# Kernel optimization log

Measured on AMD Instinct MI355X. Metric: run time of the kernel, lower is better.

Reference implementation:

```python
import jax, jax.numpy as jnp
import numpy as np
from jax import lax

D = 1024      # embed_dim
L = 8         # num_blocks
H = 8         # num_heads
P = 4         # patch_size
IMG = 64
B = 64
N = (IMG // P) ** 2 + 1   # 257 tokens (cls + patches)
DF = 4 * D
EPS = 1e-6


def _ln(x, g, b):
    m = jnp.mean(x, axis=-1, keepdims=True)
    v = jnp.var(x, axis=-1, keepdims=True)
    return (x - m) * jax.lax.rsqrt(v + EPS) * g + b


def setup_inputs() -> dict:
    key = jax.random.key(0)
    ks = jax.random.split(key, 20)
    s = 0.02
    return {
        "x": jax.random.normal(ks[0], (B, IMG, IMG, 3), jnp.float32),
        "conv_w": jax.random.normal(ks[1], (P, P, 3, D), jnp.float32) * s,
        "conv_b": jnp.zeros((D,), jnp.float32),
        "cls_token": jax.random.normal(ks[2], (1, 1, D), jnp.float32) * s,
        "pos_emb": jax.random.normal(ks[3], (N, D), jnp.float32) * s,
        "ln1_g": jnp.ones((L, D), jnp.float32),
        "ln1_b": jnp.zeros((L, D), jnp.float32),
        "wq": jax.random.normal(ks[4], (L, D, D), jnp.float32) * s,
        "wk": jax.random.normal(ks[5], (L, D, D), jnp.float32) * s,
        "wv": jax.random.normal(ks[6], (L, D, D), jnp.float32) * s,
        "proj_w": jax.random.normal(ks[7], (L, D, D), jnp.float32) * s,
        "proj_b": jnp.zeros((L, D), jnp.float32),
        "ln2_g": jnp.ones((L, D), jnp.float32),
        "ln2_b": jnp.zeros((L, D), jnp.float32),
        "mlp1_w": jax.random.normal(ks[8], (L, D, DF), jnp.float32) * s,
        "mlp1_b": jnp.zeros((L, DF), jnp.float32),
        "mlp2_w": jax.random.normal(ks[9], (L, DF, D), jnp.float32) * s,
        "mlp2_b": jnp.zeros((L, D), jnp.float32),
    }


def _forward(x, conv_w, conv_b, cls_token, pos_emb, ln1_g, ln1_b, wq, wk, wv,
             proj_w, proj_b, ln2_g, ln2_b, mlp1_w, mlp1_b, mlp2_w, mlp2_b):
    bsz = x.shape[0]
    # patch embedding: strided conv, NHWC / HWIO
    r = lax.conv_general_dilated(x, conv_w, (P, P), 'VALID',
                                 dimension_numbers=('NHWC', 'HWIO', 'NHWC')) + conv_b
    tokens = r.reshape(bsz, -1, D)                         # [B, 256, D]
    cls = jnp.broadcast_to(cls_token, (bsz, 1, D))
    t = jnp.concatenate([cls, tokens], axis=1) + pos_emb[None]   # [B, N, D]

    hd = D // H
    scale = hd ** -0.5
    for i in range(L):
        xn = _ln(t, ln1_g[i], ln1_b[i])
        q = (xn @ wq[i] * scale).reshape(bsz, N, H, hd)
        k = (xn @ wk[i]).reshape(bsz, N, H, hd)
        v = (xn @ wv[i]).reshape(bsz, N, H, hd)
        attn = jax.nn.softmax(jnp.einsum('bqhd,bkhd->bhqk', q, k), axis=-1)
        y = jnp.einsum('bhqk,bkhd->bqhd', attn, v).reshape(bsz, N, D)
        t = t + y @ proj_w[i] + proj_b[i]
        xn2 = _ln(t, ln2_g[i], ln2_b[i])
        h = jax.nn.gelu(xn2 @ mlp1_w[i] + mlp1_b[i], approximate=False)
        t = t + h @ mlp2_w[i] + mlp2_b[i]
    return t[:, 0]   # gp='none' -> cls token


def reference(x, conv_w, conv_b, cls_token, pos_emb, ln1_g, ln1_b, wq, wk, wv,
              proj_w, proj_b, ln2_g, ln2_b, mlp1_w, mlp1_b, mlp2_w, mlp2_b):
    return _forward(x, conv_w, conv_b, cls_token, pos_emb, ln1_g, ln1_b, wq, wk, wv,
                    proj_w, proj_b, ln2_g, ln2_b, mlp1_w, mlp1_b, mlp2_w, mlp2_b)
```

## Files before the change

### kernel.cpp

```cpp
#include <hip/hip_runtime.h>
#include <math.h>

typedef __bf16 bf16;
typedef __bf16 bf16x8 __attribute__((ext_vector_type(8)));
typedef __bf16 bf16x2v __attribute__((ext_vector_type(2)));
typedef float f32x4 __attribute__((ext_vector_type(4)));

#define DD     1024
#define NL     8
#define NTOK   257
#define NB     64
#define DFF    4096
#define MM     (NB*NTOK)
#define NP     288
#define HD     128
#define CHUNK  128

__device__ __forceinline__ void gld16(const void* g, void* l) {
  __builtin_amdgcn_global_load_lds((__attribute__((address_space(1))) void*)g,
                                   (__attribute__((address_space(3))) void*)l,
                                   16, 0, 0);
}

template<int NT, int NR>
__device__ __forceinline__ void stage_sw(const bf16* __restrict__ p, int ld,
                                         int row0, int rmax, int k0,
                                         char* lds, int t) {
  int wb = (t >> 6) << 10;
  int cs = ((((t & 3) - (t >> 3)) & 3) << 3);
  #pragma unroll
  for (int i = 0; i < (NR*4)/NT; ++i) {
    int r = row0 + i*(NT/4) + (t >> 2);
    r = r < rmax ? r : rmax;
    gld16(p + (long)r*ld + k0 + cs, lds + i*(NT*16) + wb);
  }
}

__device__ __forceinline__ void swz_xy(int& X, int& Y) {
  int gx = gridDim.x, gy = gridDim.y;
  int G = gx * gy;
  int orig = blockIdx.y * gx + blockIdx.x;
  int q = G >> 3, r = G & 7;
  int xcd = orig & 7, j = orig >> 3;
  int wg = (xcd < r ? xcd*(q+1) : r*(q+1) + (xcd-r)*q) + j;
  X = wg / gy; Y = wg - (wg / gy) * gy;
}

__device__ __forceinline__ void frag_mfma(const char* cA, const char* cB,
                                          int wr, int wc, int ro, int soff,
                                          f32x4 acc[4][4]) {
  bf16x8 af[4], bfr[4];
  #pragma unroll
  for (int i = 0; i < 4; ++i)
    af[i]  = *(const bf16x8*)(cA + (wr + i*16 + ro)*64 + soff);
  #pragma unroll
  for (int j = 0; j < 4; ++j)
    bfr[j] = *(const bf16x8*)(cB + (wc + j*16 + ro)*64 + soff);
  #pragma unroll
  for (int i = 0; i < 4; ++i)
    #pragma unroll
    for (int j = 0; j < 4; ++j)
      acc[i][j] = __builtin_amdgcn_mfma_f32_16x16x32_bf16(af[i], bfr[j], acc[i][j], 0, 0, 0);
}

template<int NT, int BN>
__device__ __forceinline__ void gemm_core(const bf16* __restrict__ A, int lda, int ar0, int armax,
                                          const bf16* __restrict__ Bt, int ldb, int br0, int brmax,
                                          int K, f32x4 acc[4][4], char* lds) {
  int t = threadIdx.x;
  int lane = t & 63, w = t >> 6;
  int wr = (NT == 256 ? (w >> 1) : (w >> 2)) << 6;
  int wc = (NT == 256 ? (w & 1)  : (w & 3))  << 6;
  int ro = lane & 15, q = lane >> 4;
  int soff = ((q + (ro >> 1)) & 3) << 4;
  constexpr int AB = 128*64;
  constexpr int BB = BN*64;
  char* lB = lds + 2*AB;

  stage_sw<NT,128>(A,  lda, ar0, armax, 0, lds, t);
  stage_sw<NT,BN> (Bt, ldb, br0, brmax, 0, lB,  t);
  __syncthreads();
  int cur = 0;
  for (int k0 = 32; k0 < K; k0 += 32) {
    stage_sw<NT,128>(A,  lda, ar0, armax, k0, lds + (cur^1)*AB, t);
    stage_sw<NT,BN> (Bt, ldb, br0, brmax, k0, lB  + (cur^1)*BB, t);
    frag_mfma(lds + cur*AB, lB + cur*BB, wr, wc, ro, soff, acc);
    __syncthreads();
    cur ^= 1;
  }
  frag_mfma(lds + cur*AB, lB + cur*BB, wr, wc, ro, soff, acc);
}

#define ACC_INIT f32x4 acc[4][4]; { f32x4 z = {0.f,0.f,0.f,0.f}; \
  for (int i=0;i<4;i++) for (int j=0;j<4;j++) acc[i][j]=z; }

#define EPILOG_IDX(NT) int te = threadIdx.x; int lane_ = te & 63; int w_ = te >> 6; \
  int r0 = ((NT==256 ? (w_>>1) : (w_>>2)) << 6) + ((lane_ >> 4) << 2); \
  int c0 = ((NT==256 ? (w_&1)  : (w_&3))  << 6) + (lane_ & 15);

__device__ __forceinline__ void gemm_core256(const bf16* __restrict__ A, int lda, int ar0, int armax,
                                             const bf16* __restrict__ Bt, int ldb, int br0, int brmax,
                                             int K, f32x4 acc[8][4], char* lds) {
  int t = threadIdx.x;
  int lane = t & 63, w = t >> 6;
  int wr = (w >> 2) << 7;
  int wc = (w & 3) << 6;
  int ro = lane & 15, q = lane >> 4;
  int soff = ((q + (ro >> 1)) & 3) << 4;
  int wb = w << 10;
  int cs = ((((t & 3) - (t >> 3)) & 3) << 3);

  const bf16 *pA0, *pA1, *pB0, *pB1;
  {
    int r;
    r = ar0 + (t >> 2);       r = r < armax ? r : armax;  pA0 = A  + (long)r*lda + cs;
    r = ar0 + 128 + (t >> 2); r = r < armax ? r : armax;  pA1 = A  + (long)r*lda + cs;
    r = br0 + (t >> 2);       r = r < brmax ? r : brmax;  pB0 = Bt + (long)r*ldb + cs;
    r = br0 + 128 + (t >> 2); r = r < brmax ? r : brmax;  pB1 = Bt + (long)r*ldb + cs;
  }

  int nk = K >> 5;
  auto stage = [&](int ks) {
    char* sA = lds + ((ks & 3) << 15);
    char* sB = sA + 16384;
    int k0 = ks << 5;
    gld16(pA0 + k0, sA + wb);
    gld16(pA1 + k0, sA + 8192 + wb);
    gld16(pB0 + k0, sB + wb);
    gld16(pB1 + k0, sB + 8192 + wb);
  };

  stage(0); stage(1); stage(2);
  for (int ks = 0; ks < nk; ++ks) {
    int rem = nk - 1 - ks;
    if (rem >= 2)      asm volatile("s_waitcnt vmcnt(8)" ::: "memory");
    else if (rem == 1) asm volatile("s_waitcnt vmcnt(4)" ::: "memory");
    else               asm volatile("s_waitcnt vmcnt(0)" ::: "memory");
    __builtin_amdgcn_sched_barrier(0);
    __builtin_amdgcn_s_barrier();
    __builtin_amdgcn_sched_barrier(0);
    if (ks + 3 < nk) stage(ks + 3);
    char* sA = lds + ((ks & 3) << 15);
    char* sB = sA + 16384;
    bf16x8 af[8], bfr[4];
    #pragma unroll
    for (int i = 0; i < 8; ++i)
      af[i]  = *(const bf16x8*)(sA + (wr + i*16 + ro)*64 + soff);
    #pragma unroll
    for (int j = 0; j < 4; ++j)
      bfr[j] = *(const bf16x8*)(sB + (wc + j*16 + ro)*64 + soff);
    __builtin_amdgcn_s_setprio(1);
    #pragma unroll
    for (int i = 0; i < 8; ++i)
      #pragma unroll
      for (int j = 0; j < 4; ++j)
        acc[i][j] = __builtin_amdgcn_mfma_f32_16x16x32_bf16(af[i], bfr[j], acc[i][j], 0, 0, 0);
    __builtin_amdgcn_s_setprio(0);
  }
}

#define ACC_INIT256 f32x4 acc[8][4]; { f32x4 z = {0.f,0.f,0.f,0.f}; \
  for (int i=0;i<8;i++) for (int j=0;j<4;j++) acc[i][j]=z; }

#define EPILOG_IDX256 int te = threadIdx.x; int lane_ = te & 63; int w_ = te >> 6; \
  int r0 = ((w_ >> 2) << 7) + ((lane_ >> 4) << 2); \
  int c0 = ((w_ & 3) << 6) + (lane_ & 15);

__global__ void __launch_bounds__(512, 2) k_gemm_qkv(const bf16* __restrict__ A,
    const bf16* __restrict__ Bt, bf16* __restrict__ qb, bf16* __restrict__ kb,
    bf16* __restrict__ vT) {
  __shared__ char lds[131072];
  int X, Y; swz_xy(X, Y);
  ACC_INIT256;
  gemm_core256(A, DD, X*256, MM-1, Bt, DD, Y*256, 3071, DD, acc, lds);
  EPILOG_IDX256;
  int mb = X*256, nb = Y*256;
  #pragma unroll
  for (int i=0;i<8;i++)
    #pragma unroll
    for (int r=0;r<4;r++) {
      int m = mb + r0 + i*16 + r;
      if (m < MM) {
        unsigned bb = (unsigned)m / NTOK;
        int tok = m - (int)bb*NTOK;
        #pragma unroll
        for (int j=0;j<4;j++) {
          int n = nb + c0 + j*16;
          bf16 val = (bf16)acc[i][j][r];
          if (n < 2048) {
            (n < 1024 ? qb : kb)[(long)m*DD + (n & 1023)] = val;
          } else {
            int nv = n - 2048, h = nv >> 7, d = nv & 127;
            vT[(((long)(bb*8+h))*HD + d)*NP + tok] = val;
          }
        }
      }
    }
}

__global__ void __launch_bounds__(512, 2) k_gemm_resid(const bf16* __restrict__ A,
    const bf16* __restrict__ Bt, const float* __restrict__ bias,
    float* __restrict__ T, int K) {
  __shared__ char lds[131072];
  int X, Y; swz_xy(X, Y);
  ACC_INIT256;
  gemm_core256(A, K, X*256, MM-1, Bt, K, Y*256, 1023, K, acc, lds);
  EPILOG_IDX256;
  int mb = X*256, nb = Y*256;
  #pragma unroll
  for (int i=0;i<8;i++)
    #pragma unroll
    for (int r=0;r<4;r++) {
      int m = mb + r0 + i*16 + r;
      if (m < MM) {
        #pragma unroll
        for (int j=0;j<4;j++) {
          int n = nb + c0 + j*16;
          long idx = (long)m*DD + n;
          T[idx] = T[idx] + acc[i][j][r] + bias[n];
        }
      }
    }
}

__global__ void __launch_bounds__(512, 2) k_gemm_gelu(const bf16* __restrict__ A,
    const bf16* __restrict__ Bt, const float* __restrict__ bias,
    bf16* __restrict__ Hb) {
  __shared__ char lds[131072];
  int X, Y; swz_xy(X, Y);
  ACC_INIT256;
  gemm_core256(A, DD, X*256, MM-1, Bt, DD, Y*256, 4095, DD, acc, lds);
  EPILOG_IDX256;
  int mb = X*256, nb = Y*256;
  #pragma unroll
  for (int i=0;i<8;i++)
    #pragma unroll
    for (int r=0;r<4;r++) {
      int m = mb + r0 + i*16 + r;
      if (m < MM) {
        #pragma unroll
        for (int j=0;j<4;j++) {
          int n = nb + c0 + j*16;
          float vv = acc[i][j][r] + bias[n];
          float ge = 0.5f*vv*(1.f + erff(vv*0.70710678118654752f));
          Hb[(long)m*DFF + n] = (bf16)ge;
        }
      }
    }
}

__global__ void __launch_bounds__(256) k_attn_s(const bf16* __restrict__ q,
    const bf16* __restrict__ kk, bf16* __restrict__ P, int bh0) {
  __shared__ char lds[2*8192 + 2*8192];
  int l = blockIdx.z; int bh = bh0 + l; int b = bh >> 3; int h = bh & 7;
  const bf16* Ab = q  + (long)b*NTOK*DD + h*HD;
  const bf16* Bb = kk + (long)b*NTOK*DD + h*HD;
  ACC_INIT;
  gemm_core<256,128>(Ab, DD, blockIdx.x*128, NTOK-1, Bb, DD, blockIdx.y*128, NTOK-1, HD, acc, lds);
  EPILOG_IDX(256);
  bf16* Pp = P + (long)l*NP*NP;
  int mb = blockIdx.x*128, nb = blockIdx.y*128;
  #pragma unroll
  for (int i=0;i<4;i++)
    #pragma unroll
    for (int r=0;r<4;r++) {
      int m = mb + r0 + i*16 + r;
      if (m < NTOK) {
        #pragma unroll
        for (int j=0;j<4;j++) {
          int n = nb + c0 + j*16;
          if (n < NTOK) Pp[(long)m*NP + n] = (bf16)acc[i][j][r];
        }
      }
    }
}

__global__ void __launch_bounds__(256) k_attn_pv(const bf16* __restrict__ P,
    const bf16* __restrict__ vT, bf16* __restrict__ y, int bh0) {
  __shared__ char lds[2*8192 + 2*8192];
  int l = blockIdx.z; int bh = bh0 + l; int b = bh >> 3; int h = bh & 7;
  const bf16* Ab = P  + (long)l*NP*NP;
  const bf16* Bb = vT + (long)bh*HD*NP;
  ACC_INIT;
  gemm_core<256,128>(Ab, NP, blockIdx.x*128, NP-1, Bb, NP, 0, HD-1, NP, acc, lds);
  EPILOG_IDX(256);
  int mb = blockIdx.x*128;
  #pragma unroll
  for (int i=0;i<4;i++)
    #pragma unroll
    for (int r=0;r<4;r++) {
      int m = mb + r0 + i*16 + r;
      if (m < NTOK) {
        #pragma unroll
        for (int j=0;j<4;j++) {
          int n = c0 + j*16;
          y[((long)b*NTOK + m)*DD + h*HD + n] = (bf16)acc[i][j][r];
        }
      }
    }
}

__global__ void __launch_bounds__(256) k_ln(const float* __restrict__ T,
    const float* __restrict__ g, const float* __restrict__ be,
    bf16* __restrict__ out) {
  int row = blockIdx.x;
  const float4* x4 = (const float4*)(T + (long)row*DD);
  int t = threadIdx.x;
  float4 v = x4[t];
  float s  = v.x+v.y+v.z+v.w;
  float ss = v.x*v.x+v.y*v.y+v.z*v.z+v.w*v.w;
  #pragma unroll
  for (int o=32;o;o>>=1){ s += __shfl_down(s,o); ss += __shfl_down(ss,o); }
  __shared__ float rsum[4], rsq[4];
  int lane = t&63, w = t>>6;
  if (lane==0){ rsum[w]=s; rsq[w]=ss; }
  __syncthreads();
  float S  = rsum[0]+rsum[1]+rsum[2]+rsum[3];
  float SS = rsq[0]+rsq[1]+rsq[2]+rsq[3];
  float mean = S*(1.f/DD);
  float var  = SS*(1.f/DD) - mean*mean;
  float rs = rsqrtf(var + 1e-6f);
  float4 gg = ((const float4*)g)[t];
  float4 bb = ((const float4*)be)[t];
  bf16* o = out + (long)row*DD + t*4;
  o[0]=(bf16)((v.x-mean)*rs*gg.x+bb.x);
  o[1]=(bf16)((v.y-mean)*rs*gg.y+bb.y);
  o[2]=(bf16)((v.z-mean)*rs*gg.z+bb.z);
  o[3]=(bf16)((v.w-mean)*rs*gg.w+bb.w);
}

__global__ void __launch_bounds__(256) k_softmax(bf16* __restrict__ P) {
  int t = threadIdx.x, lane = t & 63, w = t >> 6;
  int row = blockIdx.x*4 + w;
  int l = row / NTOK, qq = row - l*NTOK;
  bf16* p = P + (long)l*NP*NP + (long)qq*NP;
  float v[5]; float mx = -1e30f;
  #pragma unroll
  for (int i=0;i<5;i++){
    int c = lane + i*64;
    v[i] = (c < NTOK) ? (float)p[c] : -1e30f;
    mx = fmaxf(mx, v[i]);
  }
  #pragma unroll
  for (int o=32;o;o>>=1) mx = fmaxf(mx, __shfl_xor(mx, o));
  float s = 0.f;
  #pragma unroll
  for (int i=0;i<5;i++){ v[i] = __expf(v[i]-mx); s += v[i]; }
  #pragma unroll
  for (int o=32;o;o>>=1) s += __shfl_xor(s, o);
  float inv = 1.f / s;
  #pragma unroll
  for (int i=0;i<5;i++){ int c = lane + i*64; if (c < NTOK) p[c] = (bf16)(v[i]*inv); }
  if (lane < NP-NTOK) p[NTOK+lane] = (bf16)0.f;
}

__global__ void __launch_bounds__(256) k_transpose64(const float* __restrict__ in,
    bf16* __restrict__ out, int R, int C, float scale) {
  __shared__ float tile[64][65];
  int c0 = blockIdx.x*64, r0 = blockIdx.y*64;
  int t = threadIdx.x;
  int tr = t >> 5, tc = (t & 31) * 2;
  #pragma unroll
  for (int i = 0; i < 8; ++i) {
    int r = r0 + tr + i*8;
    float2 v = *(const float2*)&in[(long)r*C + c0 + tc];
    tile[tr + i*8][tc] = v.x; tile[tr + i*8][tc+1] = v.y;
  }
  __syncthreads();
  #pragma unroll
  for (int i = 0; i < 8; ++i) {
    int c = c0 + tr + i*8;
    bf16x2v o;
    o.x = (bf16)(tile[tc  ][tr + i*8] * scale);
    o.y = (bf16)(tile[tc+1][tr + i*8] * scale);
    *(bf16x2v*)&out[(long)c*R + r0 + tc] = o;
  }
}

__global__ void __launch_bounds__(256) k_embed(const float* __restrict__ x,
    const float* __restrict__ cw, const float* __restrict__ cb,
    const float* __restrict__ cls, const float* __restrict__ pos,
    float* __restrict__ T) {
  int blk = blockIdx.x; int b = blk / NTOK, tok = blk - b*NTOK;
  long orow = (long)(b*NTOK + tok)*DD;
  int t = threadIdx.x;
  if (tok == 0) {
    #pragma unroll
    for (int i=0;i<4;i++){ int d=t+i*256; T[orow+d] = cls[d] + pos[d]; }
    return;
  }
  __shared__ float patch[48];
  int pi = tok-1, py = pi>>4, px = pi&15;
  if (t < 48) {
    int i = t/12, j = (t/3)&3, c = t%3;
    patch[t] = x[(((long)(b*64 + py*4 + i))*64 + px*4 + j)*3 + c];
  }
  __syncthreads();
  float a[4];
  #pragma unroll
  for (int i=0;i<4;i++) a[i] = cb[t+i*256];
  for (int p=0;p<48;p++){
    float pv = patch[p];
    const float* wrow = cw + p*DD;
    #pragma unroll
    for (int i=0;i<4;i++) a[i] += pv * wrow[t+i*256];
  }
  #pragma unroll
  for (int i=0;i<4;i++){ int d=t+i*256; T[orow+d] = a[i] + pos[(long)tok*DD+d]; }
}

__global__ void __launch_bounds__(256) k_out(const float* __restrict__ T,
                                             float* __restrict__ out) {
  int b = blockIdx.x, t = threadIdx.x;
  #pragma unroll
  for (int i=0;i<4;i++){
    int d = t + i*256;
    out[(long)b*DD + d] = T[(long)b*NTOK*DD + d];
  }
}

extern "C" void kernel_launch(void* const* d_in, const int* in_sizes, int n_in,
                              void* d_out, int out_size, void* d_ws, size_t ws_size,
                              hipStream_t stream) {
  const float* x      = (const float*)d_in[0];
  const float* conv_w = (const float*)d_in[1];
  const float* conv_b = (const float*)d_in[2];
  const float* cls    = (const float*)d_in[3];
  const float* pos    = (const float*)d_in[4];
  const float* ln1_g  = (const float*)d_in[5];
  const float* ln1_b  = (const float*)d_in[6];
  const float* wq     = (const float*)d_in[7];
  const float* wk     = (const float*)d_in[8];
  const float* wv     = (const float*)d_in[9];
  const float* proj_w = (const float*)d_in[10];
  const float* proj_b = (const float*)d_in[11];
  const float* ln2_g  = (const float*)d_in[12];
  const float* ln2_b  = (const float*)d_in[13];
  const float* mlp1_w = (const float*)d_in[14];
  const float* mlp1_b = (const float*)d_in[15];
  const float* mlp2_w = (const float*)d_in[16];
  const float* mlp2_b = (const float*)d_in[17];

  const size_t TBUF_OFF = 0;
  const size_t XN_OFF   = 67371008;
  const size_t C_OFF    = XN_OFF + 33685504;
  const size_t NEED     = C_OFF + 151519232;
  if (ws_size < NEED) return;

  char* base = (char*)d_ws;
  float* tbuf  = (float*)(base + TBUF_OFF);
  bf16*  xn    = (bf16*)(base + XN_OFF);
  char*  C     = base + C_OFF;
  bf16* wqkvT  = (bf16*)(C + 0);
  bf16* projT  = wqkvT;
  bf16* qb     = (bf16*)(C + 6291456);
  bf16* kb     = (bf16*)(C + 39976960);
  bf16* vT     = (bf16*)(C + 73662464);
  bf16* Pc     = (bf16*)(C + 111411200);
  bf16* m1T    = (bf16*)(C + 0);
  bf16* m2T    = (bf16*)(C + 8388608);
  bf16* hb     = (bf16*)(C + 16777216);

  const float qscale = 0.08838834764831845f;

  k_embed<<<MM, 256, 0, stream>>>(x, conv_w, conv_b, cls, pos, tbuf);

  for (int i = 0; i < NL; ++i) {
    const long wo = (long)i*DD*DD;
    k_transpose64<<<dim3(16,16), 256, 0, stream>>>(wq + wo, wqkvT,             DD, DD, qscale);
    k_transpose64<<<dim3(16,16), 256, 0, stream>>>(wk + wo, wqkvT + 1024*1024, DD, DD, 1.f);
    k_transpose64<<<dim3(16,16), 256, 0, stream>>>(wv + wo, wqkvT + 2*1024*1024, DD, DD, 1.f);
    k_ln<<<MM, 256, 0, stream>>>(tbuf, ln1_g + i*DD, ln1_b + i*DD, xn);
    k_gemm_qkv<<<dim3(65,12), 512, 0, stream>>>(xn, wqkvT, qb, kb, vT);
    k_transpose64<<<dim3(16,16), 256, 0, stream>>>(proj_w + wo, projT, DD, DD, 1.f);
    for (int c = 0; c < 512/CHUNK; ++c) {
      k_attn_s <<<dim3(3,3,CHUNK), 256, 0, stream>>>(qb, kb, Pc, c*CHUNK);
      k_softmax<<<(CHUNK*NTOK)/4, 256, 0, stream>>>(Pc);
      k_attn_pv<<<dim3(3,1,CHUNK), 256, 0, stream>>>(Pc, vT, xn, c*CHUNK);
    }
    k_gemm_resid<<<dim3(65,4), 512, 0, stream>>>(xn, projT, proj_b + i*DD, tbuf, DD);
    k_ln<<<MM, 256, 0, stream>>>(tbuf, ln2_g + i*DD, ln2_b + i*DD, xn);
    k_transpose64<<<dim3(64,16), 256, 0, stream>>>(mlp1_w + (long)i*DD*DFF, m1T, DD, DFF, 1.f);
    k_transpose64<<<dim3(16,64), 256, 0, stream>>>(mlp2_w + (long)i*DFF*DD, m2T, DFF, DD, 1.f);
    k_gemm_gelu <<<dim3(65,16), 512, 0, stream>>>(xn, m1T, mlp1_b + i*DFF, hb);
    k_gemm_resid<<<dim3(65,4),  512, 0, stream>>>(hb, m2T, mlp2_b + i*DD, tbuf, DFF);
  }

  k_out<<<NB, 256, 0, stream>>>(tbuf, (float*)d_out);
}
```

Before: 8.137 ms.

## Split GEMM mainloop into two half-phases and use 256x128 tiles for residual GEMMs

The GEMM core is templated on tile shape and restructured so each K-step is split into two halves. A and B stages are issued separately, one between each barrier, so LDS fragment reads, global-to-LDS loads and MFMA groups interleave more finely with a prefetch depth of two. The residual GEMMs (proj and mlp2, N=1024) now use 256x128 tiles with twice as many workgroups and less LDS, giving more blocks to spread over the CUs. The cost is an extra barrier per K-step and more fiddly vmcnt accounting.

```diff
diff --git a/kernel.cpp b/kernel.cpp
--- a/kernel.cpp
+++ b/kernel.cpp
@@ -45,6 +45,10 @@
   int wg = (xcd < r ? xcd*(q+1) : r*(q+1) + (xcd-r)*q) + j;
   X = wg / gy; Y = wg - (wg / gy) * gy;
 }
+
+#define BARRIER() do { __builtin_amdgcn_sched_barrier(0); \
+  asm volatile("s_barrier" ::: "memory"); \
+  __builtin_amdgcn_sched_barrier(0); } while(0)
 
 __device__ __forceinline__ void frag_mfma(const char* cA, const char* cB,
                                           int wr, int wc, int ro, int soff,
@@ -98,69 +102,98 @@
   int r0 = ((NT==256 ? (w_>>1) : (w_>>2)) << 6) + ((lane_ >> 4) << 2); \
   int c0 = ((NT==256 ? (w_&1)  : (w_&3))  << 6) + (lane_ & 15);
 
-__device__ __forceinline__ void gemm_core256(const bf16* __restrict__ A, int lda, int ar0, int armax,
-                                             const bf16* __restrict__ Bt, int ldb, int br0, int brmax,
-                                             int K, f32x4 acc[8][4], char* lds) {
+template<int AM, int BN>
+__device__ __forceinline__ void gemm_pipe(const bf16* __restrict__ A, int lda, int ar0, int armax,
+                                          const bf16* __restrict__ Bt, int ldb, int br0, int brmax,
+                                          int K, f32x4 acc[AM/32][BN/64], char* lds) {
+  constexpr int MF = AM/32;
+  constexpr int NF = BN/64;
+  constexpr int ASLOT = AM*64;
+  constexpr int BSLOT = BN*64;
+  constexpr int LA = AM/128;
+  constexpr int LB = BN/128;
+  constexpr int NW = LA+LB;
   int t = threadIdx.x;
   int lane = t & 63, w = t >> 6;
-  int wr = (w >> 2) << 7;
-  int wc = (w & 3) << 6;
+  int wr = (w >> 2) * (AM/2);
+  int wc = (w & 3) * (BN/4);
   int ro = lane & 15, q = lane >> 4;
   int soff = ((q + (ro >> 1)) & 3) << 4;
   int wb = w << 10;
   int cs = ((((t & 3) - (t >> 3)) & 3) << 3);
-
-  const bf16 *pA0, *pA1, *pB0, *pB1;
-  {
-    int r;
-    r = ar0 + (t >> 2);       r = r < armax ? r : armax;  pA0 = A  + (long)r*lda + cs;
-    r = ar0 + 128 + (t >> 2); r = r < armax ? r : armax;  pA1 = A  + (long)r*lda + cs;
-    r = br0 + (t >> 2);       r = r < brmax ? r : brmax;  pB0 = Bt + (long)r*ldb + cs;
-    r = br0 + 128 + (t >> 2); r = r < brmax ? r : brmax;  pB1 = Bt + (long)r*ldb + cs;
-  }
-
+  char* lA = lds;
+  char* lB = lds + 4*ASLOT;
   int nk = K >> 5;
-  auto stage = [&](int ks) {
-    char* sA = lds + ((ks & 3) << 15);
-    char* sB = sA + 16384;
-    int k0 = ks << 5;
-    gld16(pA0 + k0, sA + wb);
-    gld16(pA1 + k0, sA + 8192 + wb);
-    gld16(pB0 + k0, sB + wb);
-    gld16(pB1 + k0, sB + 8192 + wb);
+
+  const bf16* pA[LA]; const bf16* pB[LB];
+  #pragma unroll
+  for (int i = 0; i < LA; ++i) {
+    int r = ar0 + i*128 + (t >> 2); r = r < armax ? r : armax;
+    pA[i] = A + (long)r*lda + cs;
+  }
+  #pragma unroll
+  for (int i = 0; i < LB; ++i) {
+    int r = br0 + i*128 + (t >> 2); r = r < brmax ? r : brmax;
+    pB[i] = Bt + (long)r*ldb + cs;
+  }
+  auto stageA = [&](int ks) {
+    char* d = lA + (ks & 3)*ASLOT + wb; int k0 = ks << 5;
+    #pragma unroll
+    for (int i = 0; i < LA; ++i) gld16(pA[i] + k0, d + i*8192);
   };
-
-  stage(0); stage(1); stage(2);
+  auto stageB = [&](int ks) {
+    char* d = lB + (ks & 3)*BSLOT + wb; int k0 = ks << 5;
+    #pragma unroll
+    for (int i = 0; i < LB; ++i) gld16(pB[i] + k0, d + i*8192);
+  };
+
+  stageA(0); stageB(0); stageA(1); stageB(1);
+  if constexpr (NW == 4) asm volatile("s_waitcnt vmcnt(4)" ::: "memory");
+  else                   asm volatile("s_waitcnt vmcnt(3)" ::: "memory");
+  BARRIER();
+
   for (int ks = 0; ks < nk; ++ks) {
-    int rem = nk - 1 - ks;
-    if (rem >= 2)      asm volatile("s_waitcnt vmcnt(8)" ::: "memory");
-    else if (rem == 1) asm volatile("s_waitcnt vmcnt(4)" ::: "memory");
-    else               asm volatile("s_waitcnt vmcnt(0)" ::: "memory");
-    __builtin_amdgcn_sched_barrier(0);
-    __builtin_amdgcn_s_barrier();
-    __builtin_amdgcn_sched_barrier(0);
-    if (ks + 3 < nk) stage(ks + 3);
-    char* sA = lds + ((ks & 3) << 15);
-    char* sB = sA + 16384;
-    bf16x8 af[8], bfr[4];
-    #pragma unroll
-    for (int i = 0; i < 8; ++i)
-      af[i]  = *(const bf16x8*)(sA + (wr + i*16 + ro)*64 + soff);
-    #pragma unroll
-    for (int j = 0; j < 4; ++j)
-      bfr[j] = *(const bf16x8*)(sB + (wc + j*16 + ro)*64 + soff);
+    char* sA = lA + (ks & 3)*ASLOT;
+    char* sB = lB + (ks & 3)*BSLOT;
+    bf16x8 af[MF], bfr[NF];
+    #pragma unroll
+    for (int f = 0; f < MF/2; ++f)
+      af[f] = *(const bf16x8*)(sA + (wr + f*16 + ro)*64 + soff);
+    #pragma unroll
+    for (int g = 0; g < NF; ++g)
+      bfr[g] = *(const bf16x8*)(sB + (wc + g*16 + ro)*64 + soff);
+    if (ks + 2 < nk) stageA(ks + 2);
+    BARRIER();
     __builtin_amdgcn_s_setprio(1);
     #pragma unroll
-    for (int i = 0; i < 8; ++i)
+    for (int f = 0; f < MF/2; ++f)
       #pragma unroll
-      for (int j = 0; j < 4; ++j)
-        acc[i][j] = __builtin_amdgcn_mfma_f32_16x16x32_bf16(af[i], bfr[j], acc[i][j], 0, 0, 0);
+      for (int g = 0; g < NF; ++g)
+        acc[f][g] = __builtin_amdgcn_mfma_f32_16x16x32_bf16(af[f], bfr[g], acc[f][g], 0, 0, 0);
     __builtin_amdgcn_s_setprio(0);
-  }
-}
-
-#define ACC_INIT256 f32x4 acc[8][4]; { f32x4 z = {0.f,0.f,0.f,0.f}; \
-  for (int i=0;i<8;i++) for (int j=0;j<4;j++) acc[i][j]=z; }
+    #pragma unroll
+    for (int f = MF/2; f < MF; ++f)
+      af[f] = *(const bf16x8*)(sA + (wr + f*16 + ro)*64 + soff);
+    if (ks + 2 < nk) stageB(ks + 2);
+    if (ks < nk - 2) {
+      if constexpr (NW == 4) asm volatile("s_waitcnt vmcnt(4)" ::: "memory");
+      else                   asm volatile("s_waitcnt vmcnt(3)" ::: "memory");
+    } else if (ks == nk - 2) {
+      asm volatile("s_waitcnt vmcnt(0)" ::: "memory");
+    }
+    BARRIER();
+    __builtin_amdgcn_s_setprio(1);
+    #pragma unroll
+    for (int f = MF/2; f < MF; ++f)
+      #pragma unroll
+      for (int g = 0; g < NF; ++g)
+        acc[f][g] = __builtin_amdgcn_mfma_f32_16x16x32_bf16(af[f], bfr[g], acc[f][g], 0, 0, 0);
+    __builtin_amdgcn_s_setprio(0);
+  }
+}
+
+#define ACC_INIT_P(MF,NF) f32x4 acc[MF][NF]; { f32x4 z = {0.f,0.f,0.f,0.f}; \
+  for (int i=0;i<MF;i++) for (int j=0;j<NF;j++) acc[i][j]=z; }
 
 #define EPILOG_IDX256 int te = threadIdx.x; int lane_ = te & 63; int w_ = te >> 6; \
   int r0 = ((w_ >> 2) << 7) + ((lane_ >> 4) << 2); \
@@ -171,8 +204,8 @@
     bf16* __restrict__ vT) {
   __shared__ char lds[131072];
   int X, Y; swz_xy(X, Y);
-  ACC_INIT256;
-  gemm_core256(A, DD, X*256, MM-1, Bt, DD, Y*256, 3071, DD, acc, lds);
+  ACC_INIT_P(8,4);
+  gemm_pipe<256,256>(A, DD, X*256, MM-1, Bt, DD, Y*256, 3071, DD, acc, lds);
   EPILOG_IDX256;
   int mb = X*256, nb = Y*256;
   #pragma unroll
@@ -201,12 +234,14 @@
 __global__ void __launch_bounds__(512, 2) k_gemm_resid(const bf16* __restrict__ A,
     const bf16* __restrict__ Bt, const float* __restrict__ bias,
     float* __restrict__ T, int K) {
-  __shared__ char lds[131072];
+  __shared__ char lds[98304];
   int X, Y; swz_xy(X, Y);
-  ACC_INIT256;
-  gemm_core256(A, K, X*256, MM-1, Bt, K, Y*256, 1023, K, acc, lds);
-  EPILOG_IDX256;
-  int mb = X*256, nb = Y*256;
+  ACC_INIT_P(8,2);
+  gemm_pipe<256,128>(A, K, X*256, MM-1, Bt, K, Y*128, 1023, K, acc, lds);
+  int te = threadIdx.x; int lane_ = te & 63; int w_ = te >> 6;
+  int r0 = ((w_ >> 2) << 7) + ((lane_ >> 4) << 2);
+  int c0 = ((w_ & 3) << 5) + (lane_ & 15);
+  int mb = X*256, nb = Y*128;
   #pragma unroll
   for (int i=0;i<8;i++)
     #pragma unroll
@@ -214,7 +249,7 @@
       int m = mb + r0 + i*16 + r;
       if (m < MM) {
         #pragma unroll
-        for (int j=0;j<4;j++) {
+        for (int j=0;j<2;j++) {
           int n = nb + c0 + j*16;
           long idx = (long)m*DD + n;
           T[idx] = T[idx] + acc[i][j][r] + bias[n];
@@ -228,8 +263,8 @@
     bf16* __restrict__ Hb) {
   __shared__ char lds[131072];
   int X, Y; swz_xy(X, Y);
-  ACC_INIT256;
-  gemm_core256(A, DD, X*256, MM-1, Bt, DD, Y*256, 4095, DD, acc, lds);
+  ACC_INIT_P(8,4);
+  gemm_pipe<256,256>(A, DD, X*256, MM-1, Bt, DD, Y*256, 4095, DD, acc, lds);
   EPILOG_IDX256;
   int mb = X*256, nb = Y*256;
   #pragma unroll
@@ -478,12 +513,12 @@
       k_softmax<<<(CHUNK*NTOK)/4, 256, 0, stream>>>(Pc);
       k_attn_pv<<<dim3(3,1,CHUNK), 256, 0, stream>>>(Pc, vT, xn, c*CHUNK);
     }
-    k_gemm_resid<<<dim3(65,4), 512, 0, stream>>>(xn, projT, proj_b + i*DD, tbuf, DD);
+    k_gemm_resid<<<dim3(65,8), 512, 0, stream>>>(xn, projT, proj_b + i*DD, tbuf, DD);
     k_ln<<<MM, 256, 0, stream>>>(tbuf, ln2_g + i*DD, ln2_b + i*DD, xn);
     k_transpose64<<<dim3(64,16), 256, 0, stream>>>(mlp1_w + (long)i*DD*DFF, m1T, DD, DFF, 1.f);
     k_transpose64<<<dim3(16,64), 256, 0, stream>>>(mlp2_w + (long)i*DFF*DD, m2T, DFF, DD, 1.f);
     k_gemm_gelu <<<dim3(65,16), 512, 0, stream>>>(xn, m1T, mlp1_b + i*DFF, hb);
-    k_gemm_resid<<<dim3(65,4),  512, 0, stream>>>(hb, m2T, mlp2_b + i*DD, tbuf, DFF);
+    k_gemm_resid<<<dim3(65,8),  512, 0, stream>>>(hb, m2T, mlp2_b + i*DD, tbuf, DFF);
   }
 
   k_out<<<NB, 256, 0, stream>>>(tbuf, (float*)d_out);
```

Result: no change. 8.083 ms (-0.7%).
